# Optimization experiments

Hardware: AMD Instinct MI355X
Metric: run time of the kernel (lower is better)

The kernel has to match this reference:

```python
import jax, jax.numpy as jnp
import numpy as np

B, S, NH, HD = 2, 4096, 16, 64


def setup_inputs() -> dict:
    key = jax.random.key(0)
    kq, kk, kv = jax.random.split(key, 3)
    q = jax.random.normal(kq, (B, S, NH, HD), dtype=jnp.float32)
    k = jax.random.normal(kk, (B, S, NH, HD), dtype=jnp.float32)
    v = jax.random.normal(kv, (B, S, NH, HD), dtype=jnp.float32)
    return {"q": q, "k": k, "v": v}


def reference(q, k, v):
    # SDPA.__call__ with attention_mask=None, segment_ids=None, is_causal=True, dropout=identity
    q_len, nheads, kv_len = q.shape[-3], q.shape[-2], k.shape[-3]
    qs = q / jnp.sqrt(jnp.asarray(q.shape[-1], q.dtype))
    scores = jnp.einsum('...tnh,...snh->...tns', qs, k)  # [B, q, nheads, kv]
    # causal mask: tril over (q, kv), broadcast over heads axis (-2)
    causal = jnp.tril(jnp.ones((q_len, kv_len), dtype=jnp.bool_))[:, None, :]
    neg_inf = jnp.finfo(scores.dtype).min
    scores = jnp.where(causal, scores, neg_inf)
    weights = jax.nn.softmax(scores.astype(jnp.float32), axis=-1).astype(scores.dtype)
    attn = jnp.einsum('...tns,...snh->...tnh', weights, v)
    return attn
```

## Files before the change

kernel.cpp:

```cpp
#include <hip/hip_runtime.h>


constexpr int BATCH  = 2;
constexpr int SEQ    = 4096;
constexpr int NHEADS = 16;
constexpr int HDIM   = 64;
constexpr int ROWSTR = NHEADS * HDIM;
constexpr int BM     = 128;
constexpr int BN     = 64;
constexpr int QTILES = SEQ / BM;
constexpr int BH     = BATCH * NHEADS;

typedef __attribute__((ext_vector_type(8)))  short v8s;
typedef __attribute__((ext_vector_type(16))) float v16f;
typedef __attribute__((ext_vector_type(4)))  unsigned int v4u;
typedef __attribute__((ext_vector_type(2)))  unsigned int v2u;

__device__ __forceinline__ unsigned pkbf(float a, float b) {
#if __has_builtin(__builtin_amdgcn_cvt_pk_bf16_f32)
    return __builtin_bit_cast(unsigned, __builtin_amdgcn_cvt_pk_bf16_f32(a, b));
#else
    unsigned ua = __float_as_uint(a); ua += 0x7FFFu + ((ua >> 16) & 1u);
    unsigned ub = __float_as_uint(b); ub += 0x7FFFu + ((ub >> 16) & 1u);
    return (ua >> 16) | (ub & 0xFFFF0000u);
#endif
}

__device__ __forceinline__ int fswz(int r) { return (r & 7) ^ ((r >> 3) & 3); }

__device__ __forceinline__ void async16(const unsigned short* g, unsigned short* l) {
    __builtin_amdgcn_global_load_lds(
        (const __attribute__((address_space(1))) unsigned int*)g,
        (__attribute__((address_space(3))) unsigned int*)l, 16, 0, 0);
}

__global__ __launch_bounds__(256, 2)
void prep(const float* __restrict__ kf, const float* __restrict__ vf,
          unsigned short* __restrict__ kb, unsigned short* __restrict__ vt)
{
    __shared__ unsigned int lds[32 * 512];
    const int tid = threadIdx.x;
    const int blk = (int)blockIdx.x;

    {
        const float4* src = (const float4*)kf + (size_t)blk * 8192;
        unsigned int* dst = (unsigned int*)kb + (size_t)blk * 16384;
        #pragma unroll 4
        for (int i = 0; i < 32; ++i) {
            const int n = i * 256 + tid;
            float4 f = src[n];
            *(v2u*)(dst + (size_t)n * 2) = (v2u){pkbf(f.x, f.y), pkbf(f.z, f.w)};
        }
    }

    const int b  = blk >> 7;
    const int s0 = (blk & 127) * 32;
    {
        const float4* src = (const float4*)vf + (size_t)(b * SEQ + s0) * 256;
        #pragma unroll 4
        for (int i = 0; i < 32; ++i) {
            float4 f = src[(size_t)i * 256 + tid];
            const int p = tid ^ (i & 15);
            *(v2u*)&lds[i * 512 + p * 2] = (v2u){pkbf(f.x, f.y), pkbf(f.z, f.w)};
        }
    }
    __syncthreads();
    {
        const int h   = tid >> 4;
        const int hd0 = (tid & 15) * 4;
        const int bh  = b * NHEADS + h;
        unsigned int* ob = (unsigned int*)vt + ((size_t)bh * HDIM + hd0) * (SEQ / 2) + (s0 >> 1);
        #pragma unroll
        for (int sc = 0; sc < 4; ++sc) {
            v2u d[8];
            #pragma unroll
            for (int j = 0; j < 8; ++j) {
                const int s = sc * 8 + j;
                d[j] = *(const v2u*)&lds[s * 512 + (tid ^ (s & 15)) * 2];
            }
            v4u w0, w1, w2, w3;
            #pragma unroll
            for (int jj = 0; jj < 4; ++jj) {
                const v2u a = d[2*jj], c = d[2*jj+1];
                w0[jj] = (a.x & 0xFFFFu) | (c.x << 16);
                w1[jj] = (a.x >> 16)     | (c.x & 0xFFFF0000u);
                w2[jj] = (a.y & 0xFFFFu) | (c.y << 16);
                w3[jj] = (a.y >> 16)     | (c.y & 0xFFFF0000u);
            }
            *(v4u*)(ob + 0 * (SEQ/2) + sc*4) = w0;
            *(v4u*)(ob + 1 * (SEQ/2) + sc*4) = w1;
            *(v4u*)(ob + 2 * (SEQ/2) + sc*4) = w2;
            *(v4u*)(ob + 3 * (SEQ/2) + sc*4) = w3;
        }
    }
}

__global__ __launch_bounds__(256, 4)
void fa_fwd(const float* __restrict__ qf, const unsigned short* __restrict__ kb,
            const unsigned short* __restrict__ vt, float* __restrict__ og)
{
    __shared__ __align__(16) unsigned short k_s[2][64 * 64];
    __shared__ __align__(16) unsigned short v_s[2][64 * 64];
    __shared__ float l_buf[BM];

    const int tid  = threadIdx.x;
    const int wave = tid >> 6;
    const int lane = tid & 63;
    const int hh   = lane >> 5;
    const int l32  = lane & 31;

    const int n  = (int)blockIdx.x;
    const int qtile = QTILES - 1 - (n >> 5);
    const int bh = n & 31;
    const int b = bh >> 4, h = bh & 15;
    const int qbase = qtile * BM;
    const int jmax  = 2 * qtile + 2;

    const int lrow  = lane >> 3;
    const int lcol8 = (lane & 7) ^ lrow ^ wave;
    const int fx = (l32 & 7) ^ ((l32 >> 3) & 3);

    {
        const int krow = tid >> 2;
        const int kc   = (tid & 3) * 16;
        const int sg0  = (2 * (tid & 3))     ^ fswz(krow);
        const int sg1  = (2 * (tid & 3) + 1) ^ fswz(krow);
        const float sc = 0.125f * 1.44269504088896340736f;
        #pragma unroll
        for (int half = 0; half < 2; ++half) {
            const float4* src = (const float4*)(qf +
                ((size_t)((b * SEQ + qbase + half * 64 + krow) * NHEADS + h)) * HDIM + kc);
            float4 f0 = src[0], f1 = src[1], f2 = src[2], f3 = src[3];
            unsigned short* dst = half ? &v_s[0][krow * 64] : &k_s[0][krow * 64];
            *(v4u*)&dst[sg0 * 8] = (v4u){pkbf(f0.x*sc, f0.y*sc), pkbf(f0.z*sc, f0.w*sc),
                                         pkbf(f1.x*sc, f1.y*sc), pkbf(f1.z*sc, f1.w*sc)};
            *(v4u*)&dst[sg1 * 8] = (v4u){pkbf(f2.x*sc, f2.y*sc), pkbf(f2.z*sc, f2.w*sc),
                                         pkbf(f3.x*sc, f3.y*sc), pkbf(f3.z*sc, f3.w*sc)};
        }
    }
    __syncthreads();
    v8s bq[4];
    {
        const int R = wave * 32 + l32;
        const unsigned short* qrow = (R < 64) ? &k_s[0][R * 64] : &v_s[0][(R - 64) * 64];
        #pragma unroll
        for (int c = 0; c < 4; ++c)
            bq[c] = *(const v8s*)&qrow[(((2*c + hh) ^ fswz(R & 63)) * 8)];
    }
    __syncthreads();

    const unsigned short* kgb = kb + (size_t)b * SEQ * ROWSTR + (size_t)h * HDIM;
    const unsigned short* vgb = vt + (size_t)bh * HDIM * SEQ;

    #pragma unroll
    for (int i = 0; i < 2; ++i) {
        const int rbase = i * 32 + wave * 8;
        async16(kgb + (size_t)(rbase + lrow) * ROWSTR + lcol8 * 8, &k_s[0][rbase * 64]);
        async16(vgb + (size_t)(rbase + lrow) * SEQ    + lcol8 * 8, &v_s[0][rbase * 64]);
    }

    v16f o_acc[2];
    o_acc[0] = (v16f)(0.f); o_acc[1] = (v16f)(0.f);
    float l_lane = 0.f;
    const int q_abs = qbase + wave * 32 + l32;

    for (int jt = 0; jt < jmax; ++jt) {
        const int buf = jt & 1;
        __syncthreads();

        if (jt + 1 < jmax) {
            const int nb  = (jt + 1) & 1;
            const int kb2 = (jt + 1) * BN;
            #pragma unroll
            for (int i = 0; i < 2; ++i) {
                const int rbase = i * 32 + wave * 8;
                async16(kgb + (size_t)(kb2 + rbase + lrow) * ROWSTR + lcol8 * 8, &k_s[nb][rbase * 64]);
                async16(vgb + (size_t)(rbase + lrow) * SEQ + kb2    + lcol8 * 8, &v_s[nb][rbase * 64]);
            }
        }

        v16f sacc[2];
        sacc[0] = (v16f)(0.f); sacc[1] = (v16f)(0.f);
        #pragma unroll
        for (int mt = 0; mt < 2; ++mt) {
            const int r = mt * 32 + l32;
            #pragma unroll
            for (int c = 0; c < 4; ++c) {
                v8s ak = *(const v8s*)&k_s[buf][r * 64 + (((2*c + hh) ^ fx) * 8)];
                sacc[mt] = __builtin_amdgcn_mfma_f32_32x32x16_bf16(ak, bq[c], sacc[mt], 0, 0, 0);
            }
        }

        const bool masked = (jt >= jmax - 2);
        v8s pf[4];
        #pragma unroll
        for (int mt = 0; mt < 2; ++mt) {
            #pragma unroll
            for (int r = 0; r < 16; ++r) {
                float pv = __builtin_amdgcn_exp2f(sacc[mt][r]);
                if (masked) {
                    const int k_abs = jt * 64 + mt * 32 + (r & 3) + 8 * (r >> 2) + 4 * hh;
                    pv = (k_abs > q_abs) ? 0.f : pv;
                }
                sacc[mt][r] = pv;
                l_lane += pv;
            }
            #pragma unroll
            for (int cc = 0; cc < 2; ++cc) {
                const unsigned lo0 = pkbf(sacc[mt][8*cc+0], sacc[mt][8*cc+1]);
                const unsigned lo1 = pkbf(sacc[mt][8*cc+2], sacc[mt][8*cc+3]);
                const unsigned hi0 = pkbf(sacc[mt][8*cc+4], sacc[mt][8*cc+5]);
                const unsigned hi1 = pkbf(sacc[mt][8*cc+6], sacc[mt][8*cc+7]);
                const unsigned s0 = hh ? lo0 : hi0;
                const unsigned s1 = hh ? lo1 : hi1;
                const unsigned t0 = (unsigned)__shfl_xor((int)s0, 32, 64);
                const unsigned t1 = (unsigned)__shfl_xor((int)s1, 32, 64);
                v4u w;
                w.x = hh ? t0 : lo0;
                w.y = hh ? t1 : lo1;
                w.z = hh ? hi0 : t0;
                w.w = hh ? hi1 : t1;
                pf[mt*2 + cc] = __builtin_bit_cast(v8s, w);
            }
        }

        #pragma unroll
        for (int nt = 0; nt < 2; ++nt) {
            const int r = nt * 32 + l32;
            #pragma unroll
            for (int c = 0; c < 4; ++c) {
                v8s bv = *(const v8s*)&v_s[buf][r * 64 + (((2*c + hh) ^ fx) * 8)];
                o_acc[nt] = __builtin_amdgcn_mfma_f32_32x32x16_bf16(pf[c], bv, o_acc[nt], 0, 0, 0);
            }
        }
    }

    const float lt = l_lane + __shfl_xor(l_lane, 32);
    if (hh == 0) l_buf[wave * 32 + l32] = lt;
    __syncthreads();

    #pragma unroll
    for (int r = 0; r < 16; ++r) {
        const int q_local = (r & 3) + 8 * (r >> 2) + 4 * hh;
        const float inv_l = 1.0f / l_buf[wave * 32 + q_local];
        const int qrow = qbase + wave * 32 + q_local;
        float* dst = og + ((size_t)((b * SEQ + qrow) * NHEADS + h)) * HDIM + l32;
        dst[0]  = o_acc[0][r] * inv_l;
        dst[32] = o_acc[1][r] * inv_l;
    }
}

extern "C" void kernel_launch(void* const* d_in, const int* in_sizes, int n_in,
                              void* d_out, int out_size, void* d_ws, size_t ws_size,
                              hipStream_t stream) {
    const float* q = (const float*)d_in[0];
    const float* k = (const float*)d_in[1];
    const float* v = (const float*)d_in[2];
    float* out = (float*)d_out;

    const size_t TEN = (size_t)BATCH * NHEADS * SEQ * HDIM;
    unsigned short* kbuf = (unsigned short*)d_ws;
    unsigned short* vbuf = kbuf + TEN;

    prep<<<256, 256, 0, stream>>>(k, v, kbuf, vbuf);
    fa_fwd<<<QTILES * BH, 256, 0, stream>>>(q, kbuf, vbuf, out);
}
```

Before: 252.3 us.

## Split prep into more blocks, use permlane32 swap and MFMA row sums

The prep kernel is split into 1024 blocks for the K conversion and 1024 blocks that transpose V per head and sequence tile, using a padded LDS layout. This gives more parallelism and fewer bank conflicts than the old 256-block version. In the attention kernel, the cross-half shuffle that builds the P operand is replaced by permlane32_swap where the builtin exists. The softmax row sum now comes from an extra MFMA against a ones vector instead of per-lane adds, a shuffle and an LDS round-trip. This adds MFMA work per tile, and the sum is taken over bf16-rounded probabilities.

```diff
diff --git a/kernel.cpp b/kernel.cpp
--- a/kernel.cpp
+++ b/kernel.cpp
@@ -34,64 +34,61 @@
         (__attribute__((address_space(3))) unsigned int*)l, 16, 0, 0);
 }
 
-__global__ __launch_bounds__(256, 2)
+__global__ __launch_bounds__(256, 4)
 void prep(const float* __restrict__ kf, const float* __restrict__ vf,
           unsigned short* __restrict__ kb, unsigned short* __restrict__ vt)
 {
-    __shared__ unsigned int lds[32 * 512];
+    __shared__ unsigned int lds[128 * 33];
     const int tid = threadIdx.x;
     const int blk = (int)blockIdx.x;
 
-    {
-        const float4* src = (const float4*)kf + (size_t)blk * 8192;
-        unsigned int* dst = (unsigned int*)kb + (size_t)blk * 16384;
-        #pragma unroll 4
-        for (int i = 0; i < 32; ++i) {
+    if (blk < 1024) {
+        const float4* src = (const float4*)kf + (size_t)blk * 2048;
+        unsigned int* dst = (unsigned int*)kb + (size_t)blk * 4096;
+        #pragma unroll
+        for (int i = 0; i < 8; ++i) {
             const int n = i * 256 + tid;
             float4 f = src[n];
             *(v2u*)(dst + (size_t)n * 2) = (v2u){pkbf(f.x, f.y), pkbf(f.z, f.w)};
         }
-    }
-
-    const int b  = blk >> 7;
-    const int s0 = (blk & 127) * 32;
-    {
-        const float4* src = (const float4*)vf + (size_t)(b * SEQ + s0) * 256;
-        #pragma unroll 4
-        for (int i = 0; i < 32; ++i) {
-            float4 f = src[(size_t)i * 256 + tid];
-            const int p = tid ^ (i & 15);
-            *(v2u*)&lds[i * 512 + p * 2] = (v2u){pkbf(f.x, f.y), pkbf(f.z, f.w)};
+        return;
+    }
+
+    const int t  = blk - 1024;
+    const int b  = t >> 9;
+    const int h  = (t >> 5) & 15;
+    const int s0 = (t & 31) * 128;
+
+    {
+        const float4* vff = (const float4*)vf + (size_t)b * SEQ * 256;
+        const int c2 = (tid & 15) * 2;
+        #pragma unroll
+        for (int i = 0; i < 8; ++i) {
+            const int srow = i * 16 + (tid >> 4);
+            float4 f = vff[(size_t)(s0 + srow) * 256 + h * 16 + (tid & 15)];
+            lds[srow * 33 + c2]     = pkbf(f.x, f.y);
+            lds[srow * 33 + c2 + 1] = pkbf(f.z, f.w);
         }
     }
     __syncthreads();
     {
-        const int h   = tid >> 4;
-        const int hd0 = (tid & 15) * 4;
-        const int bh  = b * NHEADS + h;
-        unsigned int* ob = (unsigned int*)vt + ((size_t)bh * HDIM + hd0) * (SEQ / 2) + (s0 >> 1);
-        #pragma unroll
-        for (int sc = 0; sc < 4; ++sc) {
-            v2u d[8];
-            #pragma unroll
-            for (int j = 0; j < 8; ++j) {
-                const int s = sc * 8 + j;
-                d[j] = *(const v2u*)&lds[s * 512 + (tid ^ (s & 15)) * 2];
-            }
-            v4u w0, w1, w2, w3;
-            #pragma unroll
-            for (int jj = 0; jj < 4; ++jj) {
-                const v2u a = d[2*jj], c = d[2*jj+1];
-                w0[jj] = (a.x & 0xFFFFu) | (c.x << 16);
-                w1[jj] = (a.x >> 16)     | (c.x & 0xFFFF0000u);
-                w2[jj] = (a.y & 0xFFFFu) | (c.y << 16);
-                w3[jj] = (a.y >> 16)     | (c.y & 0xFFFF0000u);
-            }
-            *(v4u*)(ob + 0 * (SEQ/2) + sc*4) = w0;
-            *(v4u*)(ob + 1 * (SEQ/2) + sc*4) = w1;
-            *(v4u*)(ob + 2 * (SEQ/2) + sc*4) = w2;
-            *(v4u*)(ob + 3 * (SEQ/2) + sc*4) = w3;
-        }
+        const int w    = tid >> 6;
+        const int lane = tid & 63;
+        const int sh   = (lane & 1) * 16;
+        const unsigned int* lcol = &lds[w * 32 * 33 + (lane >> 1)];
+        unsigned int out[16];
+        #pragma unroll
+        for (int j = 0; j < 16; ++j) {
+            const unsigned a = lcol[(2 * j)     * 33];
+            const unsigned c = lcol[(2 * j + 1) * 33];
+            out[j] = ((a >> sh) & 0xFFFFu) | (((c >> sh) & 0xFFFFu) << 16);
+        }
+        unsigned int* dst = (unsigned int*)vt
+            + ((size_t)((b * NHEADS + h) * HDIM + lane)) * (SEQ / 2)
+            + ((s0 + w * 32) >> 1);
+        #pragma unroll
+        for (int j = 0; j < 4; ++j)
+            *(v4u*)(dst + 4 * j) = (v4u){out[4*j], out[4*j+1], out[4*j+2], out[4*j+3]};
     }
 }
 
@@ -101,7 +98,6 @@
 {
     __shared__ __align__(16) unsigned short k_s[2][64 * 64];
     __shared__ __align__(16) unsigned short v_s[2][64 * 64];
-    __shared__ float l_buf[BM];
 
     const int tid  = threadIdx.x;
     const int wave = tid >> 6;
@@ -159,9 +155,12 @@
         async16(vgb + (size_t)(rbase + lrow) * SEQ    + lcol8 * 8, &v_s[0][rbase * 64]);
     }
 
+    const short ONE = (short)0x3F80;
+    const v8s bones = {ONE, ONE, ONE, ONE, ONE, ONE, ONE, ONE};
+
     v16f o_acc[2];
     o_acc[0] = (v16f)(0.f); o_acc[1] = (v16f)(0.f);
-    float l_lane = 0.f;
+    v16f l_acc = (v16f)(0.f);
     const int q_abs = qbase + wave * 32 + l32;
 
     for (int jt = 0; jt < jmax; ++jt) {
@@ -203,7 +202,6 @@
                     pv = (k_abs > q_abs) ? 0.f : pv;
                 }
                 sacc[mt][r] = pv;
-                l_lane += pv;
             }
             #pragma unroll
             for (int cc = 0; cc < 2; ++cc) {
@@ -211,6 +209,11 @@
                 const unsigned lo1 = pkbf(sacc[mt][8*cc+2], sacc[mt][8*cc+3]);
                 const unsigned hi0 = pkbf(sacc[mt][8*cc+4], sacc[mt][8*cc+5]);
                 const unsigned hi1 = pkbf(sacc[mt][8*cc+6], sacc[mt][8*cc+7]);
+#if __has_builtin(__builtin_amdgcn_permlane32_swap)
+                auto r0 = __builtin_amdgcn_permlane32_swap(lo0, hi0, false, false);
+                auto r1 = __builtin_amdgcn_permlane32_swap(lo1, hi1, false, false);
+                pf[mt*2 + cc] = __builtin_bit_cast(v8s, (v4u){r0[0], r1[0], r0[1], r1[1]});
+#else
                 const unsigned s0 = hh ? lo0 : hi0;
                 const unsigned s1 = hh ? lo1 : hi1;
                 const unsigned t0 = (unsigned)__shfl_xor((int)s0, 32, 64);
@@ -221,6 +224,7 @@
                 w.z = hh ? hi0 : t0;
                 w.w = hh ? hi1 : t1;
                 pf[mt*2 + cc] = __builtin_bit_cast(v8s, w);
+#endif
             }
         }
 
@@ -233,16 +237,16 @@
                 o_acc[nt] = __builtin_amdgcn_mfma_f32_32x32x16_bf16(pf[c], bv, o_acc[nt], 0, 0, 0);
             }
         }
-    }
-
-    const float lt = l_lane + __shfl_xor(l_lane, 32);
-    if (hh == 0) l_buf[wave * 32 + l32] = lt;
-    __syncthreads();
+
+        #pragma unroll
+        for (int c = 0; c < 4; ++c)
+            l_acc = __builtin_amdgcn_mfma_f32_32x32x16_bf16(pf[c], bones, l_acc, 0, 0, 0);
+    }
 
     #pragma unroll
     for (int r = 0; r < 16; ++r) {
         const int q_local = (r & 3) + 8 * (r >> 2) + 4 * hh;
-        const float inv_l = 1.0f / l_buf[wave * 32 + q_local];
+        const float inv_l = 1.0f / l_acc[r];
         const int qrow = qbase + wave * 32 + q_local;
         float* dst = og + ((size_t)((b * SEQ + qrow) * NHEADS + h)) * HDIM + l32;
         dst[0]  = o_acc[0][r] * inv_l;
@@ -262,6 +266,6 @@
     unsigned short* kbuf = (unsigned short*)d_ws;
     unsigned short* vbuf = kbuf + TEN;
 
-    prep<<<256, 256, 0, stream>>>(k, v, kbuf, vbuf);
+    prep<<<2048, 256, 0, stream>>>(k, v, kbuf, vbuf);
     fa_fwd<<<QTILES * BH, 256, 0, stream>>>(q, kbuf, vbuf, out);
 }
```

Measured after the change: 265.9 us. +5.4%, slower.
